# Kernel tuning notes

Hardware: AMD Instinct MI355X
Metric: run time of the kernel (lower is better)

Reference implementation:

```python
import jax, jax.numpy as jnp
import numpy as np

EMBED_DIM = 1024
NUM_HEADS = 16
HEAD_DIM = EMBED_DIM // NUM_HEADS


def setup_inputs() -> dict:
    key = jax.random.key(0)
    k_x, k_qw, k_qb, k_ow, k_ob = jax.random.split(key, 5)
    B, T, C = 4, 2048, EMBED_DIM
    s = 1.0 / np.sqrt(C)
    return {
        "x": jax.random.normal(k_x, (B, T, C), dtype=jnp.float32),
        # torch nn.Linear weights: [out_features, in_features]
        "qkv_w": jax.random.uniform(k_qw, (3 * C, C), jnp.float32, -s, s),
        "qkv_b": jax.random.uniform(k_qb, (3 * C,), jnp.float32, -s, s),
        "out_w": jax.random.uniform(k_ow, (C, C), jnp.float32, -s, s),
        "out_b": jax.random.uniform(k_ob, (C,), jnp.float32, -s, s),
    }


def reference(x, qkv_w, qkv_b, out_w, out_b):
    B, T, C = x.shape
    H, D = NUM_HEADS, HEAD_DIM
    qkv = x @ qkv_w.T + qkv_b                      # [B,T,3C]
    qkv = qkv.reshape(B, T, 3, H, D).transpose(2, 0, 3, 1, 4)  # [3,B,H,T,D]
    Q, K, V = qkv[0], qkv[1], qkv[2]
    scores = jnp.einsum("bhtd,bhsd->bhts", Q, K) / np.sqrt(D).astype(np.float32)
    causal = jnp.triu(jnp.ones((T, T), dtype=bool), k=1)        # mask future
    scores = jnp.where(causal, -jnp.inf, scores)
    attn_weights = jax.nn.softmax(scores, axis=-1)              # [B,H,T,T]
    out = jnp.einsum("bhts,bhsd->bhtd", attn_weights, V)
    out = out.transpose(0, 2, 1, 3).reshape(B, T, C)
    return out @ out_w.T + out_b, attn_weights
```

## Files before the change

### kernel.cpp

```cpp
#include <hip/hip_runtime.h>
#include <cstdint>
#include <cstddef>

#define Bq  4
#define Tq  2048
#define Cq  1024
#define Hq  16
#define Dq  64
#define BTq 8192
#define C3q 3072

using bf16x8 = __attribute__((ext_vector_type(8))) short;
using f32x4  = __attribute__((ext_vector_type(4))) float;
using us4    = __attribute__((ext_vector_type(4))) unsigned short;

__device__ __forceinline__ unsigned short f2bf(float f) {
  unsigned u = __builtin_bit_cast(unsigned, f);
  return (unsigned short)((u + 0x7fffu + ((u >> 16) & 1u)) >> 16);
}
__device__ __forceinline__ float bf2f(unsigned short h) {
  return __builtin_bit_cast(float, (unsigned)h << 16);
}

__device__ __forceinline__ void gload_lds16(const void* g, void* l) {
  __builtin_amdgcn_global_load_lds(
      (const __attribute__((address_space(1))) void*)g,
      (__attribute__((address_space(3))) void*)l, 16, 0, 0);
}

__device__ __forceinline__ void swz_tile(int gx, int gy, int& bx, int& by) {
  const int GROUP = 8;
  int nwg = gx * gy;
  int raw = blockIdx.x + gx * blockIdx.y;
  int id  = (raw & 7) * (nwg >> 3) + (raw >> 3);
  int per = GROUP * gx;
  int grp = id / per;
  int rem = id - grp * per;
  int first = grp * GROUP;
  int gsz = (gy - first < GROUP) ? (gy - first) : GROUP;
  by = first + rem % gsz;
  bx = rem / gsz;
}

__global__ __launch_bounds__(256) void cvt3_kernel(
    const float* __restrict__ s0, unsigned short* __restrict__ d0, int n0,
    const float* __restrict__ s1, unsigned short* __restrict__ d1, int n1,
    const float* __restrict__ s2, unsigned short* __restrict__ d2, int n2) {
  int i = blockIdx.x * 256 + threadIdx.x;
  int stride = gridDim.x * 256;
  int ntot = n0 + n1 + n2;
  for (; i < ntot; i += stride) {
    const float* src; unsigned short* dst; int j = i;
    if (j < n0) { src = s0; dst = d0; }
    else if ((j -= n0) < n1) { src = s1; dst = d1; }
    else { j -= n1; src = s2; dst = d2; }
    float4 v = reinterpret_cast<const float4*>(src)[j];
    us4 o = { f2bf(v.x), f2bf(v.y), f2bf(v.z), f2bf(v.w) };
    reinterpret_cast<us4*>(dst)[j] = o;
  }
}

template<int EPI>
__global__ __launch_bounds__(256) void gemm128(
    const unsigned short* __restrict__ A, const unsigned short* __restrict__ Bw,
    const float* __restrict__ bias,
    unsigned short* __restrict__ Qb, unsigned short* __restrict__ Kb,
    unsigned short* __restrict__ Vtb, float* __restrict__ Cout,
    int M, int N, int K)
{
  __shared__ unsigned short As[128][32];
  __shared__ unsigned short Bs[128][32];
  int bx, by;
  swz_tile(gridDim.x, gridDim.y, bx, by);
  const int n0 = bx * 128, m0 = by * 128;
  const int tid = threadIdx.x;
  const int w = tid >> 6, l = tid & 63, r = l & 15, g = l >> 4;
  const int wm = w >> 1, wn = w & 1;
  const int ldRow = tid >> 2, ldCol = (tid & 3) * 8;
  f32x4 acc[4][4] = {};

  const unsigned short* Ar0 = A  + (size_t)(m0 +      ldRow) * K + ldCol;
  const unsigned short* Ar1 = A  + (size_t)(m0 + 64 + ldRow) * K + ldCol;
  const unsigned short* Br0 = Bw + (size_t)(n0 +      ldRow) * K + ldCol;
  const unsigned short* Br1 = Bw + (size_t)(n0 + 64 + ldRow) * K + ldCol;
  char* Ab0 = (char*)&As[0][0]        + w * 1024;
  char* Ab1 = (char*)&As[0][0] + 4096 + w * 1024;
  char* Bb0 = (char*)&Bs[0][0]        + w * 1024;
  char* Bb1 = (char*)&Bs[0][0] + 4096 + w * 1024;

  for (int k0 = 0; k0 < K; k0 += 32) {
    __syncthreads();
    gload_lds16(Ar0 + k0, Ab0);
    gload_lds16(Ar1 + k0, Ab1);
    gload_lds16(Br0 + k0, Bb0);
    gload_lds16(Br1 + k0, Bb1);
    __syncthreads();
    bf16x8 a[4], b[4];
    #pragma unroll
    for (int i = 0; i < 4; ++i) a[i] = *(const bf16x8*)&As[wm*64 + i*16 + r][g*8];
    #pragma unroll
    for (int j = 0; j < 4; ++j) b[j] = *(const bf16x8*)&Bs[wn*64 + j*16 + r][g*8];
    #pragma unroll
    for (int i = 0; i < 4; ++i)
      #pragma unroll
      for (int j = 0; j < 4; ++j)
        acc[i][j] = __builtin_amdgcn_mfma_f32_16x16x32_bf16(a[i], b[j], acc[i][j], 0, 0, 0);
  }

  if (EPI == 0) {
    const int which = n0 >> 10;
    #pragma unroll
    for (int i = 0; i < 4; ++i)
      #pragma unroll
      for (int j = 0; j < 4; ++j) {
        int gc  = n0 + wn*64 + j*16 + r;
        int gr0 = m0 + wm*64 + i*16 + 4*g;
        float bv = bias[gc];
        int hd = gc & 1023;
        int h = hd >> 6, d = hd & 63;
        if (which == 2) {
          int b = gr0 >> 11, t0 = gr0 & 2047;
          int bh = b*Hq + h;
          us4 pk = { f2bf(acc[i][j][0] + bv), f2bf(acc[i][j][1] + bv),
                     f2bf(acc[i][j][2] + bv), f2bf(acc[i][j][3] + bv) };
          *(us4*)&Vtb[(size_t)(bh*Dq + d)*Tq + t0] = pk;
        } else {
          unsigned short* dst = which ? Kb : Qb;
          #pragma unroll
          for (int jj = 0; jj < 4; ++jj) {
            int gr = gr0 + jj;
            int b = gr >> 11, t = gr & 2047;
            int bh = b*Hq + h;
            dst[(size_t)(bh*Tq + t)*Dq + d] = f2bf(acc[i][j][jj] + bv);
          }
        }
      }
  } else {
    #pragma unroll
    for (int i = 0; i < 4; ++i)
      #pragma unroll
      for (int j = 0; j < 4; ++j) {
        int gc = n0 + wn*64 + j*16 + r;
        float bv = bias[gc];
        #pragma unroll
        for (int jj = 0; jj < 4; ++jj) {
          int gr = m0 + wm*64 + i*16 + 4*g + jj;
          Cout[(size_t)gr * N + gc] = acc[i][j][jj] + bv;
        }
      }
  }
}

#define PROWB 4224
#define XMASK(row_) ((((row_) & 7) << 4) ^ ((((row_) >> 2) & 3) << 5))

__global__ __launch_bounds__(512, 4) void attn_kernel(
    const unsigned short* __restrict__ Qb, const unsigned short* __restrict__ Kb,
    const unsigned short* __restrict__ Vtb,
    float* __restrict__ attn, unsigned short* __restrict__ ctxb)
{
  __shared__ __align__(16) unsigned short P[16][2112];
  __shared__ float red[8][32];
  __shared__ float invl_s[32];

  const int raw = blockIdx.x + 64 * blockIdx.y;
  const int id  = (raw & 7) * 512 + (raw >> 3);
  const int p   = id & 63;
  const int bh  = id >> 6;

  const int tid = threadIdx.x, w = tid >> 6, l = tid & 63, r = l & 15, g = l >> 4;
  const int qbA = p * 16, qbB = (127 - p) * 16;
  const int NA = (qbA + 16 + 31) >> 5;
  const int NB = (qbB + 16 + 31) >> 5;
  const int LAc = NA * 32, LBc = NB * 32;

  const unsigned short* Qp = Qb  + (size_t)bh * Tq * Dq;
  const unsigned short* Kp = Kb  + (size_t)bh * Tq * Dq;
  const unsigned short* Vp = Vtb + (size_t)bh * Dq * Tq;
  char* Pmut = (char*)&P[0][0];

  bf16x8 aqA0 = *(const bf16x8*)&Qp[(size_t)(qbA + r)*Dq      + g*8];
  bf16x8 aqA1 = *(const bf16x8*)&Qp[(size_t)(qbA + r)*Dq + 32 + g*8];
  bf16x8 aqB0 = *(const bf16x8*)&Qp[(size_t)(qbB + r)*Dq      + g*8];
  bf16x8 aqB1 = *(const bf16x8*)&Qp[(size_t)(qbB + r)*Dq + 32 + g*8];

  float lsumA[4] = {0.f,0.f,0.f,0.f}, lsumB[4] = {0.f,0.f,0.f,0.f};

#define LOADK(ci_, D00, D01, D10, D11)                                              \
  {                                                                                 \
    int cj_ = ((ci_) < NA) ? (ci_) : (ci_) - NA;                                    \
    int k0c_ = cj_ * 32;                                                            \
    D00 = *(const bf16x8*)&Kp[(size_t)(k0c_ + r)*Dq      + g*8];                    \
    D01 = *(const bf16x8*)&Kp[(size_t)(k0c_ + r)*Dq + 32 + g*8];                    \
    D10 = *(const bf16x8*)&Kp[(size_t)(k0c_ + 16 + r)*Dq      + g*8];               \
    D11 = *(const bf16x8*)&Kp[(size_t)(k0c_ + 16 + r)*Dq + 32 + g*8];               \
  }

  {
    bf16x8 k00, k01, k10, k11, n00, n01, n10, n11;
    int ci = w;
    if (ci < 65) LOADK(ci, k00, k01, k10, k11);
    for (; ci < 65; ci += 8) {
      if (ci + 8 < 65) LOADK(ci + 8, n00, n01, n10, n11);
      const bool isA = ci < NA;
      const int cj  = isA ? ci : ci - NA;
      const int k0c = cj * 32;
      const int qb_ = isA ? qbA : qbB;
      const int cb_ = isA ? k0c : LAc + k0c;
      bf16x8 q0_ = isA ? aqA0 : aqB0;
      bf16x8 q1_ = isA ? aqA1 : aqB1;
      f32x4 z = {0.f,0.f,0.f,0.f};
      __builtin_amdgcn_s_setprio(1);
      f32x4 s0 = __builtin_amdgcn_mfma_f32_16x16x32_bf16(q0_, k00, z, 0, 0, 0);
      s0 = __builtin_amdgcn_mfma_f32_16x16x32_bf16(q1_, k01, s0, 0, 0, 0);
      f32x4 s1 = __builtin_amdgcn_mfma_f32_16x16x32_bf16(q0_, k10, z, 0, 0, 0);
      s1 = __builtin_amdgcn_mfma_f32_16x16x32_bf16(q1_, k11, s1, 0, 0, 0);
      __builtin_amdgcn_s_setprio(0);
      float tch[4];
      #pragma unroll
      for (int jj = 0; jj < 4; ++jj) {
        int q = qb_ + 4*g + jj;
        float p0 = (k0c + r      <= q) ? __expf(s0[jj]*0.125f) : 0.f;
        float p1 = (k0c + 16 + r <= q) ? __expf(s1[jj]*0.125f) : 0.f;
        tch[jj] = p0 + p1;
        int row = 4*g + jj, xm = XMASK(row);
        *(unsigned short*)(Pmut + row*PROWB + (((cb_ + r)*2)      ^ xm)) = f2bf(p0);
        *(unsigned short*)(Pmut + row*PROWB + (((cb_ + 16 + r)*2) ^ xm)) = f2bf(p1);
      }
      if (isA) { lsumA[0]+=tch[0]; lsumA[1]+=tch[1]; lsumA[2]+=tch[2]; lsumA[3]+=tch[3]; }
      else     { lsumB[0]+=tch[0]; lsumB[1]+=tch[1]; lsumB[2]+=tch[2]; lsumB[3]+=tch[3]; }
      k00 = n00; k01 = n01; k10 = n10; k11 = n11;
    }
  }

  #pragma unroll
  for (int jj = 0; jj < 4; ++jj) {
    float sa = lsumA[jj], sb = lsumB[jj];
    #pragma unroll
    for (int off = 1; off < 16; off <<= 1) {
      sa += __shfl_xor(sa, off, 64);
      sb += __shfl_xor(sb, off, 64);
    }
    if (r == 0) { red[w][4*g + jj] = sa; red[w][16 + 4*g + jj] = sb; }
  }
  __syncthreads();
  if (tid < 32) {
    float s = 0.f;
    #pragma unroll
    for (int ww = 0; ww < 8; ++ww) s += red[ww][tid];
    invl_s[tid] = 1.f / s;
  }
  __syncthreads();

  if (w < 4) {
    #pragma unroll
    for (int s = 0; s < 2; ++s) {
      const int idx   = s * 256 + tid;
      const int s16   = idx >> 8;
      const int row16 = (idx >> 4) & 15;
      const int seg   = (idx & 15) * 8;
      const int xm16  = XMASK(row16);
      const char* Prow = Pmut + row16 * PROWB;
      const int Lc    = s16 ? LBc : LAc;
      const int cbase = s16 ? LAc : 0;
      float inv = invl_s[s16*16 + row16];
      size_t ob = ((size_t)bh*Tq + (s16 ? qbB : qbA) + row16) * Tq;
      for (int cb = seg; cb < Tq; cb += 128) {
        f32x4 v0 = {0.f,0.f,0.f,0.f}, v1 = {0.f,0.f,0.f,0.f};
        if (cb < Lc) {
          bf16x8 pv = *(const bf16x8*)(Prow + (((cbase + cb)*2) ^ xm16));
          v0[0]=bf2f((unsigned short)pv[0])*inv; v0[1]=bf2f((unsigned short)pv[1])*inv;
          v0[2]=bf2f((unsigned short)pv[2])*inv; v0[3]=bf2f((unsigned short)pv[3])*inv;
          v1[0]=bf2f((unsigned short)pv[4])*inv; v1[1]=bf2f((unsigned short)pv[5])*inv;
          v1[2]=bf2f((unsigned short)pv[6])*inv; v1[3]=bf2f((unsigned short)pv[7])*inv;
        }
        __builtin_nontemporal_store(v0, (f32x4*)&attn[ob + cb]);
        __builtin_nontemporal_store(v1, (f32x4*)&attn[ob + cb + 4]);
      }
    }
  } else {
    const int dblk = w - 4;
    const char* Pr = Pmut + r * PROWB;
    const int xr = XMASK(r);
    const unsigned short* Vrow = &Vp[(size_t)(dblk*16 + r) * Tq];
    f32x4 coA0 = {0.f,0.f,0.f,0.f}, coA1 = {0.f,0.f,0.f,0.f};
    f32x4 coB0 = {0.f,0.f,0.f,0.f}, coB1 = {0.f,0.f,0.f,0.f};
    bf16x8 pa, bv, pan, bvn;
    {
      pa = *(const bf16x8*)(Pr + (((0 + g*8)*2) ^ xr));
      bv = *(const bf16x8*)&Vrow[g*8];
    }
    for (int ci = 0; ci < 65; ++ci) {
      if (ci + 1 < 65) {
        int cn = ci + 1;
        int cj = (cn < NA) ? cn : cn - NA;
        int cb = (cn < NA) ? cn*32 : LAc + cj*32;
        pan = *(const bf16x8*)(Pr + (((cb + g*8)*2) ^ xr));
        bvn = *(const bf16x8*)&Vrow[cj*32 + g*8];
      }
      if (ci < NA) {
        if (ci & 1) coA1 = __builtin_amdgcn_mfma_f32_16x16x32_bf16(pa, bv, coA1, 0, 0, 0);
        else        coA0 = __builtin_amdgcn_mfma_f32_16x16x32_bf16(pa, bv, coA0, 0, 0, 0);
      } else {
        if (ci & 1) coB1 = __builtin_amdgcn_mfma_f32_16x16x32_bf16(pa, bv, coB1, 0, 0, 0);
        else        coB0 = __builtin_amdgcn_mfma_f32_16x16x32_bf16(pa, bv, coB0, 0, 0, 0);
      }
      pa = pan; bv = bvn;
    }
    const int b = bh >> 4, h = bh & 15;
    #pragma unroll
    for (int jj = 0; jj < 4; ++jj) {
      int tA = qbA + 4*g + jj;
      ctxb[(size_t)(b*Tq + tA)*Cq + h*Dq + dblk*16 + r] =
          f2bf((coA0[jj] + coA1[jj]) * invl_s[4*g + jj]);
      int tB = qbB + 4*g + jj;
      ctxb[(size_t)(b*Tq + tB)*Cq + h*Dq + dblk*16 + r] =
          f2bf((coB0[jj] + coB1[jj]) * invl_s[16 + 4*g + jj]);
    }
  }
#undef LOADK
}

extern "C" void kernel_launch(void* const* d_in, const int* in_sizes, int n_in,
                              void* d_out, int out_size, void* d_ws, size_t ws_size,
                              hipStream_t stream) {
  const float* x     = (const float*)d_in[0];
  const float* qkv_w = (const float*)d_in[1];
  const float* qkv_b = (const float*)d_in[2];
  const float* out_w = (const float*)d_in[3];
  const float* out_b = (const float*)d_in[4];
  float* out  = (float*)d_out;
  float* attn = out + (size_t)BTq * Cq;

  char* ws = (char*)d_ws;
  unsigned short* xb    = (unsigned short*)(ws);
  unsigned short* wqkvb = (unsigned short*)(ws + (16u << 20));
  unsigned short* woutb = (unsigned short*)(ws + (22u << 20));
  unsigned short* Qb    = (unsigned short*)(ws + (24u << 20));
  unsigned short* Kb    = (unsigned short*)(ws + (40u << 20));
  unsigned short* Vtb   = (unsigned short*)(ws + (56u << 20));
  unsigned short* ctxb  = (unsigned short*)(ws + (72u << 20));

  cvt3_kernel<<<2048, 256, 0, stream>>>(
      x,     xb,    (BTq * Cq) / 4,
      qkv_w, wqkvb, (C3q * Cq) / 4,
      out_w, woutb, (Cq * Cq) / 4);

  dim3 g1(C3q / 128, BTq / 128);
  gemm128<0><<<g1, 256, 0, stream>>>(xb, wqkvb, qkv_b, Qb, Kb, Vtb, nullptr, BTq, C3q, Cq);

  dim3 g2(64, Bq * Hq);
  attn_kernel<<<g2, 512, 0, stream>>>(Qb, Kb, Vtb, attn, ctxb);

  dim3 g3(Cq / 128, BTq / 128);
  gemm128<1><<<g3, 256, 0, stream>>>(ctxb, woutb, out_b, nullptr, nullptr, nullptr, out, BTq, Cq, Cq);
}
```

Measured before the change: 510.6 us.

## Use two-pass softmax: compute row sums first, then write normalized probabilities directly

Adds a first QK^T pass that only accumulates the exp row sums. A second pass recomputes the scores, normalizes them, and stores fp32 attention weights straight to global memory from the MFMA loop. The bf16 P tile is still kept in LDS for the PV product, and four waves only zero-fill the masked tail. This drops the separate LDS readback-and-convert pass for the attention output and the final rescale of the context. The cost is a second round of QK^T MFMAs, exp and K loads, plus narrow 4-byte scattered stores instead of 16-byte vector stores.

After: 532.5 us. 1.04x slower.

```diff
diff --git a/kernel.cpp b/kernel.cpp
--- a/kernel.cpp
+++ b/kernel.cpp
@@ -184,8 +184,6 @@
   bf16x8 aqB0 = *(const bf16x8*)&Qp[(size_t)(qbB + r)*Dq      + g*8];
   bf16x8 aqB1 = *(const bf16x8*)&Qp[(size_t)(qbB + r)*Dq + 32 + g*8];
 
-  float lsumA[4] = {0.f,0.f,0.f,0.f}, lsumB[4] = {0.f,0.f,0.f,0.f};
-
 #define LOADK(ci_, D00, D01, D10, D11)                                              \
   {                                                                                 \
     int cj_ = ((ci_) < NA) ? (ci_) : (ci_) - NA;                                    \
@@ -194,6 +192,66 @@
     D01 = *(const bf16x8*)&Kp[(size_t)(k0c_ + r)*Dq + 32 + g*8];                    \
     D10 = *(const bf16x8*)&Kp[(size_t)(k0c_ + 16 + r)*Dq      + g*8];               \
     D11 = *(const bf16x8*)&Kp[(size_t)(k0c_ + 16 + r)*Dq + 32 + g*8];               \
+  }
+
+  float lsumA[4] = {0.f,0.f,0.f,0.f}, lsumB[4] = {0.f,0.f,0.f,0.f};
+  {
+    bf16x8 k00, k01, k10, k11, n00, n01, n10, n11;
+    int ci = w;
+    if (ci < 65) LOADK(ci, k00, k01, k10, k11);
+    for (; ci < 65; ci += 8) {
+      if (ci + 8 < 65) LOADK(ci + 8, n00, n01, n10, n11);
+      const bool isA = ci < NA;
+      const int k0c = (isA ? ci : ci - NA) * 32;
+      const int qb_ = isA ? qbA : qbB;
+      bf16x8 q0_ = isA ? aqA0 : aqB0;
+      bf16x8 q1_ = isA ? aqA1 : aqB1;
+      f32x4 z = {0.f,0.f,0.f,0.f};
+      __builtin_amdgcn_s_setprio(1);
+      f32x4 s0 = __builtin_amdgcn_mfma_f32_16x16x32_bf16(q0_, k00, z, 0, 0, 0);
+      s0 = __builtin_amdgcn_mfma_f32_16x16x32_bf16(q1_, k01, s0, 0, 0, 0);
+      f32x4 s1 = __builtin_amdgcn_mfma_f32_16x16x32_bf16(q0_, k10, z, 0, 0, 0);
+      s1 = __builtin_amdgcn_mfma_f32_16x16x32_bf16(q1_, k11, s1, 0, 0, 0);
+      __builtin_amdgcn_s_setprio(0);
+      float t0 = 0.f, t1 = 0.f, t2 = 0.f, t3 = 0.f;
+      #pragma unroll
+      for (int jj = 0; jj < 4; ++jj) {
+        int q = qb_ + 4*g + jj;
+        float e0 = (k0c + r      <= q) ? __expf(s0[jj]*0.125f) : 0.f;
+        float e1 = (k0c + 16 + r <= q) ? __expf(s1[jj]*0.125f) : 0.f;
+        float e = e0 + e1;
+        if (jj == 0) t0 = e; else if (jj == 1) t1 = e; else if (jj == 2) t2 = e; else t3 = e;
+      }
+      if (isA) { lsumA[0]+=t0; lsumA[1]+=t1; lsumA[2]+=t2; lsumA[3]+=t3; }
+      else     { lsumB[0]+=t0; lsumB[1]+=t1; lsumB[2]+=t2; lsumB[3]+=t3; }
+      k00 = n00; k01 = n01; k10 = n10; k11 = n11;
+    }
+  }
+
+  #pragma unroll
+  for (int jj = 0; jj < 4; ++jj) {
+    float sa = lsumA[jj], sb = lsumB[jj];
+    #pragma unroll
+    for (int off = 1; off < 16; off <<= 1) {
+      sa += __shfl_xor(sa, off, 64);
+      sb += __shfl_xor(sb, off, 64);
+    }
+    if (r == 0) { red[w][4*g + jj] = sa; red[w][16 + 4*g + jj] = sb; }
+  }
+  __syncthreads();
+  if (tid < 32) {
+    float s = 0.f;
+    #pragma unroll
+    for (int ww = 0; ww < 8; ++ww) s += red[ww][tid];
+    invl_s[tid] = 1.f / s;
+  }
+  __syncthreads();
+
+  float invA[4], invB[4];
+  #pragma unroll
+  for (int jj = 0; jj < 4; ++jj) {
+    invA[jj] = invl_s[4*g + jj];
+    invB[jj] = invl_s[16 + 4*g + jj];
   }
 
   {
@@ -216,66 +274,36 @@
       f32x4 s1 = __builtin_amdgcn_mfma_f32_16x16x32_bf16(q0_, k10, z, 0, 0, 0);
       s1 = __builtin_amdgcn_mfma_f32_16x16x32_bf16(q1_, k11, s1, 0, 0, 0);
       __builtin_amdgcn_s_setprio(0);
-      float tch[4];
       #pragma unroll
       for (int jj = 0; jj < 4; ++jj) {
-        int q = qb_ + 4*g + jj;
-        float p0 = (k0c + r      <= q) ? __expf(s0[jj]*0.125f) : 0.f;
-        float p1 = (k0c + 16 + r <= q) ? __expf(s1[jj]*0.125f) : 0.f;
-        tch[jj] = p0 + p1;
-        int row = 4*g + jj, xm = XMASK(row);
+        const int row = 4*g + jj;
+        const int q = qb_ + row;
+        float inv = isA ? invA[jj] : invB[jj];
+        float p0 = (k0c + r      <= q) ? __expf(s0[jj]*0.125f) * inv : 0.f;
+        float p1 = (k0c + 16 + r <= q) ? __expf(s1[jj]*0.125f) * inv : 0.f;
+        size_t rowb = ((size_t)bh*Tq + q)*Tq + k0c;
+        __builtin_nontemporal_store(p0, &attn[rowb + r]);
+        __builtin_nontemporal_store(p1, &attn[rowb + 16 + r]);
+        int xm = XMASK(row);
         *(unsigned short*)(Pmut + row*PROWB + (((cb_ + r)*2)      ^ xm)) = f2bf(p0);
         *(unsigned short*)(Pmut + row*PROWB + (((cb_ + 16 + r)*2) ^ xm)) = f2bf(p1);
       }
-      if (isA) { lsumA[0]+=tch[0]; lsumA[1]+=tch[1]; lsumA[2]+=tch[2]; lsumA[3]+=tch[3]; }
-      else     { lsumB[0]+=tch[0]; lsumB[1]+=tch[1]; lsumB[2]+=tch[2]; lsumB[3]+=tch[3]; }
       k00 = n00; k01 = n01; k10 = n10; k11 = n11;
     }
   }
-
-  #pragma unroll
-  for (int jj = 0; jj < 4; ++jj) {
-    float sa = lsumA[jj], sb = lsumB[jj];
-    #pragma unroll
-    for (int off = 1; off < 16; off <<= 1) {
-      sa += __shfl_xor(sa, off, 64);
-      sb += __shfl_xor(sb, off, 64);
-    }
-    if (r == 0) { red[w][4*g + jj] = sa; red[w][16 + 4*g + jj] = sb; }
-  }
   __syncthreads();
-  if (tid < 32) {
-    float s = 0.f;
-    #pragma unroll
-    for (int ww = 0; ww < 8; ++ww) s += red[ww][tid];
-    invl_s[tid] = 1.f / s;
-  }
-  __syncthreads();
 
   if (w < 4) {
-    #pragma unroll
-    for (int s = 0; s < 2; ++s) {
-      const int idx   = s * 256 + tid;
-      const int s16   = idx >> 8;
-      const int row16 = (idx >> 4) & 15;
-      const int seg   = (idx & 15) * 8;
-      const int xm16  = XMASK(row16);
-      const char* Prow = Pmut + row16 * PROWB;
-      const int Lc    = s16 ? LBc : LAc;
-      const int cbase = s16 ? LAc : 0;
-      float inv = invl_s[s16*16 + row16];
-      size_t ob = ((size_t)bh*Tq + (s16 ? qbB : qbA) + row16) * Tq;
-      for (int cb = seg; cb < Tq; cb += 128) {
-        f32x4 v0 = {0.f,0.f,0.f,0.f}, v1 = {0.f,0.f,0.f,0.f};
-        if (cb < Lc) {
-          bf16x8 pv = *(const bf16x8*)(Prow + (((cbase + cb)*2) ^ xm16));
-          v0[0]=bf2f((unsigned short)pv[0])*inv; v0[1]=bf2f((unsigned short)pv[1])*inv;
-          v0[2]=bf2f((unsigned short)pv[2])*inv; v0[3]=bf2f((unsigned short)pv[3])*inv;
-          v1[0]=bf2f((unsigned short)pv[4])*inv; v1[1]=bf2f((unsigned short)pv[5])*inv;
-          v1[2]=bf2f((unsigned short)pv[6])*inv; v1[3]=bf2f((unsigned short)pv[7])*inv;
-        }
-        __builtin_nontemporal_store(v0, (f32x4*)&attn[ob + cb]);
-        __builtin_nontemporal_store(v1, (f32x4*)&attn[ob + cb + 4]);
+    f32x4 zero4 = {0.f,0.f,0.f,0.f};
+    #pragma unroll
+    for (int rr = 0; rr < 8; ++rr) {
+      int row32 = w*8 + rr;
+      int strip = row32 >> 4, row16 = row32 & 15;
+      int start = strip ? LBc : LAc;
+      size_t ob = ((size_t)bh*Tq + (strip ? qbB : qbA) + row16) * Tq;
+      for (int c = start + l*8; c < Tq; c += 512) {
+        __builtin_nontemporal_store(zero4, (f32x4*)&attn[ob + c]);
+        __builtin_nontemporal_store(zero4, (f32x4*)&attn[ob + c + 4]);
       }
     }
   } else {
@@ -311,11 +339,9 @@
     #pragma unroll
     for (int jj = 0; jj < 4; ++jj) {
       int tA = qbA + 4*g + jj;
-      ctxb[(size_t)(b*Tq + tA)*Cq + h*Dq + dblk*16 + r] =
-          f2bf((coA0[jj] + coA1[jj]) * invl_s[4*g + jj]);
+      ctxb[(size_t)(b*Tq + tA)*Cq + h*Dq + dblk*16 + r] = f2bf(coA0[jj] + coA1[jj]);
       int tB = qbB + 4*g + jj;
-      ctxb[(size_t)(b*Tq + tB)*Cq + h*Dq + dblk*16 + r] =
-          f2bf((coB0[jj] + coB1[jj]) * invl_s[16 + 4*g + jj]);
+      ctxb[(size_t)(b*Tq + tB)*Cq + h*Dq + dblk*16 + r] = f2bf(coB0[jj] + coB1[jj]);
     }
   }
 #undef LOADK
```
